# Kernel tuning notes

Measured on AMD Instinct MI355X. Metric: run time of the kernel, lower is better.

Reference implementation:

```python
import jax, jax.numpy as jnp
import numpy as np

L, H = 6, 8          # depth, heads
DM, DH, M = 512, 64, 256  # d_model, d_head, nb random features
EPS = 1e-4


def sinusoidal_pe(n, d, dtype):
    pos = jnp.arange(n, dtype=jnp.float32)[:, None]
    div = jnp.exp(jnp.arange(0, d, 2, dtype=jnp.float32) * (-(np.log(10000.0) / d)))
    pe = jnp.zeros((n, d), jnp.float32)
    pe = pe.at[:, 0::2].set(jnp.sin(pos * div))
    pe = pe.at[:, 1::2].set(jnp.cos(pos * div))
    return pe.astype(dtype)


def layer_norm(x, g, b, eps=1e-5):
    mu = jnp.mean(x, -1, keepdims=True)
    var = jnp.mean(jnp.square(x - mu), -1, keepdims=True)
    return (x - mu) * jax.lax.rsqrt(var + eps) * g + b


def softmax_features(x, proj, is_query):
    # FAVOR+ positive softmax-kernel features. x: [b,h,n,dh], proj: [m,dh]
    dn = DH ** -0.25
    xd = x * dn
    u = jnp.einsum('bhnd,md->bhnm', xd, proj)            # [b,h,n,m]
    diag = 0.5 * jnp.sum(xd * xd, -1, keepdims=True)      # ||x||^2/2 (normalized)
    if is_query:
        stab = jnp.max(u, axis=-1, keepdims=True)
    else:
        stab = jnp.max(u, axis=(-2, -1), keepdims=True)
    return (M ** -0.5) * (jnp.exp(u - diag - stab) + EPS)


def split_heads(t, b, n):
    return t.reshape(b, n, H, DH).transpose(0, 2, 1, 3)   # [b,h,n,dh]


def reference(x, proj, ln1_g, ln1_b, wq, wk, wv, wo, bo, ln2_g, ln2_b, w1, b1, w2, b2):
    b, n, d = x.shape
    x = x + sinusoidal_pe(n, d, x.dtype)[None]
    for i in range(L):
        # --- FAVOR+ linear attention (pre-norm) ---
        h = layer_norm(x, ln1_g[i], ln1_b[i])
        q = split_heads(h @ wq[i], b, n)
        k = split_heads(h @ wk[i], b, n)
        v = split_heads(h @ wv[i], b, n)
        qp = softmax_features(q, proj[i], True)           # [b,h,n,m]
        kp = softmax_features(k, proj[i], False)
        ksum = jnp.sum(kp, axis=2)                         # [b,h,m]
        d_inv = 1.0 / jnp.einsum('bhnm,bhm->bhn', qp, ksum)
        ctx = jnp.einsum('bhnm,bhnd->bhmd', kp, v)         # [b,h,m,dh]
        o = jnp.einsum('bhnm,bhmd->bhnd', qp, ctx) * d_inv[..., None]
        o = o.transpose(0, 2, 1, 3).reshape(b, n, DM)
        x = x + o @ wo[i] + bo[i]
        # --- feed-forward (pre-norm, GELU) ---
        h = layer_norm(x, ln2_g[i], ln2_b[i])
        x = x + jax.nn.gelu(h @ w1[i] + b1[i], approximate=False) @ w2[i] + b2[i]
    return x


def setup_inputs() -> dict:
    key = jax.random.key(0)
    ks = jax.random.split(key, 9)
    s_in = DM ** -0.5
    s_ff = (4 * DM) ** -0.5
    return {
        'x':     jax.random.normal(ks[0], (8, 2048, DM), jnp.float32),
        'proj':  jax.random.normal(ks[1], (L, M, DH), jnp.float32),
        'ln1_g': jnp.ones((L, DM), jnp.float32),
        'ln1_b': jnp.zeros((L, DM), jnp.float32),
        'wq':    jax.random.normal(ks[2], (L, DM, DM), jnp.float32) * s_in,
        'wk':    jax.random.normal(ks[3], (L, DM, DM), jnp.float32) * s_in,
        'wv':    jax.random.normal(ks[4], (L, DM, DM), jnp.float32) * s_in,
        'wo':    jax.random.normal(ks[5], (L, DM, DM), jnp.float32) * s_in,
        'bo':    jnp.zeros((L, DM), jnp.float32),
        'ln2_g': jnp.ones((L, DM), jnp.float32),
        'ln2_b': jnp.zeros((L, DM), jnp.float32),
        'w1':    jax.random.normal(ks[6], (L, DM, 4 * DM), jnp.float32) * s_in,
        'b1':    jnp.zeros((L, 4 * DM), jnp.float32),
        'w2':    jax.random.normal(ks[7], (L, 4 * DM, DM), jnp.float32) * s_ff,
        'b2':    jnp.zeros((L, DM), jnp.float32),
    }
```

## Files before the change

### kernel.cpp

```cpp
#include <hip/hip_runtime.h>
#include <math.h>

#define LNUM 6
#define HNUM 8
#define DMODEL 512
#define DHEAD 64
#define MFEAT 256
#define BATCH 8
#define SEQ 2048
#define TOK (BATCH*SEQ)
#define BHN (BATCH*HNUM)
#define DFF 2048
#define EPSF 1e-4f
#define LN_EPS 1e-5f
#define DNRM 0.35355339059327373f
#define SMF 0.0625f

typedef unsigned short u16;
typedef __attribute__((ext_vector_type(8))) short bf16x8;
typedef __attribute__((ext_vector_type(4))) float f32x4;
#define MFMA16(a,b,c) __builtin_amdgcn_mfma_f32_16x16x32_bf16(a,b,c,0,0,0)

#define GLOAD16(g,l) __builtin_amdgcn_global_load_lds( \
    (const __attribute__((address_space(1))) void*)(g), \
    (__attribute__((address_space(3))) void*)(l), 16, 0, 0)

__device__ __forceinline__ u16 f2bf(float f){
  unsigned int u = __float_as_uint(f);
  u = (u + 0x7fffu + ((u >> 16) & 1u)) >> 16;
  return (u16)u;
}
__device__ __forceinline__ float bf2f(u16 s){
  return __uint_as_float(((unsigned int)s) << 16);
}
__device__ __forceinline__ void atomicMaxF(float* addr, float val){
  if(val >= 0.f) atomicMax((int*)addr, __float_as_int(val));
  else           atomicMin((unsigned int*)addr, __float_as_uint(val));
}
__device__ __forceinline__ float fast_gelu(float z){
  float g2 = z*(1.5957691216f + 0.07135481628f*z*z);
  return z / (1.0f + __expf(-g2));
}

__global__ void k_addpe(const float* __restrict__ x, float* __restrict__ xo){
  int idx = blockIdx.x*256 + threadIdx.x;
  int d = idx & (DMODEL-1);
  int n = (idx >> 9) & (SEQ-1);
  int j = d >> 1;
  float freq = expf((float)(2*j) * (-9.210340371976184f / (float)DMODEL));
  float ang = (float)n * freq;
  float pe = (d & 1) ? cosf(ang) : sinf(ang);
  xo[idx] = x[idx] + pe;
}

__global__ void k_ln(const float* __restrict__ x, const float* __restrict__ g,
                     const float* __restrict__ bv, u16* __restrict__ out){
  __shared__ float sred[8];
  int t = blockIdx.x, tid = threadIdx.x;
  const float2 v = ((const float2*)(x + (size_t)t*DMODEL))[tid];
  float s = v.x + v.y;
  #pragma unroll
  for(int o=32;o;o>>=1) s += __shfl_down(s,o);
  if((tid&63)==0) sred[tid>>6] = s;
  __syncthreads();
  if(tid==0) sred[4] = (sred[0]+sred[1]+sred[2]+sred[3]) * (1.0f/DMODEL);
  __syncthreads();
  float mu = sred[4];
  float dx = v.x - mu, dy = v.y - mu;
  float s2 = dx*dx + dy*dy;
  #pragma unroll
  for(int o=32;o;o>>=1) s2 += __shfl_down(s2,o);
  if((tid&63)==0) sred[tid>>6] = s2;
  __syncthreads();
  if(tid==0) sred[5] = rsqrtf((sred[0]+sred[1]+sred[2]+sred[3])*(1.0f/DMODEL) + LN_EPS);
  __syncthreads();
  float rs = sred[5];
  const float2 gg = ((const float2*)g)[tid];
  const float2 bb = ((const float2*)bv)[tid];
  ushort2 o2; o2.x = f2bf(dx*rs*gg.x + bb.x); o2.y = f2bf(dy*rs*gg.y + bb.y);
  ((ushort2*)(out + (size_t)t*DMODEL))[tid] = o2;
}

__global__ void k_pcvt(const float* __restrict__ p, u16* __restrict__ pb){
  int i = blockIdx.x*256 + threadIdx.x;
  pb[i] = f2bf(p[i]);
}

__global__ void k_wcvt_all(const float* __restrict__ wq, const float* __restrict__ wk,
                           const float* __restrict__ wv, const float* __restrict__ wo,
                           const float* __restrict__ w1, const float* __restrict__ w2,
                           u16* __restrict__ wqT, u16* __restrict__ wkT,
                           u16* __restrict__ wvT, u16* __restrict__ woT,
                           u16* __restrict__ w1T, u16* __restrict__ w2T,
                           float* __restrict__ ksum, float* __restrict__ kmax){
  int bid = blockIdx.x;
  if(bid >= 768){
    int i = (bid-768)*256 + threadIdx.x;
    ksum[i] = 0.f;
    if(i < BHN) kmax[i] = -INFINITY;
    return;
  }
  const float* src; u16* dst; int K, N, bx, by;
  if(bid < 256){
    int which = bid >> 6, sub = bid & 63;
    src = which==0 ? wq : which==1 ? wk : which==2 ? wv : wo;
    dst = which==0 ? wqT : which==1 ? wkT : which==2 ? wvT : woT;
    K = 512; N = 512; bx = sub & 7; by = sub >> 3;
  } else if(bid < 512){
    int sub = bid - 256; src = w1; dst = w1T; K = 512; N = 2048; bx = sub & 31; by = sub >> 5;
  } else {
    int sub = bid - 512; src = w2; dst = w2T; K = 2048; N = 512; bx = sub & 7; by = sub >> 3;
  }
  __shared__ float sm[64][65];
  int kt = by*64, nt = bx*64;
  int t = threadIdx.x, c = t & 63, r4 = t >> 6;
  #pragma unroll
  for(int i=0;i<16;i++){
    int kl = i*4 + r4;
    sm[kl][c] = src[(size_t)(kt+kl)*N + nt + c];
  }
  __syncthreads();
  #pragma unroll
  for(int i=0;i<16;i++){
    int nl = i*4 + r4;
    dst[(size_t)(nt+nl)*K + kt + c] = f2bf(sm[c][nl]);
  }
}

template<int EPI>
__global__ __launch_bounds__(256,4)
void k_mm(const u16* __restrict__ A, const u16* __restrict__ Bt,
          const float* __restrict__ bias, void* __restrict__ Cv,
          int Nc, int K){
  __shared__ u16 As[2][128*32];
  __shared__ u16 Bs[2][128*32];
  int tid = threadIdx.x;
  int w = tid >> 6, lane = tid & 63;
  int wr = w >> 1, wc = w & 1;
  int hi = lane >> 4, li = lane & 15;
  int row0 = blockIdx.y*128, col0 = blockIdx.x*128;
  int lr = lane >> 2;
  int cs = (lane & 3) ^ ((lane >> 3) & 3);
  const u16* gA = A  + (size_t)(row0 + w*16 + lr)*K + cs*8;
  const u16* gB = Bt + (size_t)(col0 + w*16 + lr)*K + cs*8;
  int rb = li*32 + ((hi ^ ((li>>1)&3))<<3);
  f32x4 acc[4][4] = {};

#define STAGE_MM(b,k0) { \
    GLOAD16(gA + (k0),                &As[b][(w*16)*32]);      \
    GLOAD16(gA + (size_t)64*K + (k0), &As[b][(64+w*16)*32]);   \
    GLOAD16(gB + (k0),                &Bs[b][(w*16)*32]);      \
    GLOAD16(gB + (size_t)64*K + (k0), &Bs[b][(64+w*16)*32]); }

  int nk = K >> 5;
  STAGE_MM(0, 0)
  STAGE_MM(1, 32)
  for(int t=0; t<nk; ++t){
    __builtin_amdgcn_sched_barrier(0);
    if(t+1 < nk){ asm volatile("s_waitcnt vmcnt(4)"); }
    else        { asm volatile("s_waitcnt vmcnt(0)"); }
    __builtin_amdgcn_s_barrier();
    __builtin_amdgcn_sched_barrier(0);
    const u16* pa = &As[t&1][0];
    const u16* pb = &Bs[t&1][0];
    bf16x8 bfr[4];
    #pragma unroll
    for(int q=0;q<4;q++) bfr[q] = *(const bf16x8*)&pb[rb + wc*2048 + q*512];
    __builtin_amdgcn_s_setprio(1);
    #pragma unroll
    for(int i2=0;i2<4;i2++){
      bf16x8 a = *(const bf16x8*)&pa[rb + wr*2048 + i2*512];
      #pragma unroll
      for(int j2=0;j2<4;j2++)
        acc[i2][j2] = MFMA16(a, bfr[j2], acc[i2][j2]);
    }
    __builtin_amdgcn_s_setprio(0);
    __builtin_amdgcn_sched_barrier(0);
    __builtin_amdgcn_s_barrier();
    __builtin_amdgcn_sched_barrier(0);
    if(t+2 < nk){ STAGE_MM(t&1, (size_t)(t+2)*32) }
  }
#undef STAGE_MM

  #pragma unroll
  for(int i2=0;i2<4;i2++){
    #pragma unroll
    for(int j2=0;j2<4;j2++){
      int col = col0 + wc*64 + j2*16 + li;
      float bcol = (EPI==2 || EPI==3) ? bias[col] : 0.f;
      if constexpr (EPI==4){
        int nb = row0 + wr*64 + i2*16 + hi*4;
        int b = nb >> 11, n = nb & (SEQ-1);
        int h = col >> 6, dh = col & 63;
        ushort4 pk;
        pk.x = f2bf(acc[i2][j2][0]); pk.y = f2bf(acc[i2][j2][1]);
        pk.z = f2bf(acc[i2][j2][2]); pk.w = f2bf(acc[i2][j2][3]);
        *(ushort4*)((u16*)Cv + (((size_t)(b*HNUM+h)*DHEAD + dh)*SEQ + n)) = pk;
      } else {
        #pragma unroll
        for(int r=0;r<4;r++){
          int row = row0 + wr*64 + i2*16 + hi*4 + r;
          float v = acc[i2][j2][r];
          if constexpr (EPI==1){
            int b = row >> 11, n = row & (SEQ-1);
            int h = col >> 6, dh = col & 63;
            ((u16*)Cv)[((size_t)(b*HNUM+h)*SEQ + n)*DHEAD + dh] = f2bf(v);
          } else if constexpr (EPI==2){
            ((float*)Cv)[(size_t)row*Nc + col] += v + bcol;
          } else {
            ((u16*)Cv)[(size_t)row*Nc + col] = f2bf(fast_gelu(v + bcol));
          }
        }
      }
    }
  }
}

template<int EPI>
__global__ __launch_bounds__(512)
void k_mm8(const u16* __restrict__ A, const u16* __restrict__ Bt,
           const float* __restrict__ bias, void* __restrict__ Cv,
           int Nc, int K){
  __shared__ u16 Ab[3][256*64];
  __shared__ u16 Bb[3][128*64];
  int tid = threadIdx.x;
  int w = tid >> 6, lane = tid & 63;
  int wr = w >> 1, wc = w & 1;
  int hi = lane >> 4, li = lane & 15;
  int row0 = blockIdx.y*256, col0 = blockIdx.x*128;
  int lr = lane >> 3;
  int lc = (lane & 7) ^ lr;
  const u16* gA = A  + (size_t)(row0 + w*8 + lr)*K + lc*8;
  const u16* gB = Bt + (size_t)(col0 + w*8 + lr)*K + lc*8;
  f32x4 acc[4][4] = {};

#define STG8(buf,k0) { \
    GLOAD16(gA + (k0),                  &Ab[buf][w*512]);          \
    GLOAD16(gA + (size_t)64*K  + (k0),  &Ab[buf][4096  + w*512]);  \
    GLOAD16(gA + (size_t)128*K + (k0),  &Ab[buf][8192  + w*512]);  \
    GLOAD16(gA + (size_t)192*K + (k0),  &Ab[buf][12288 + w*512]);  \
    GLOAD16(gB + (k0),                  &Bb[buf][w*512]);          \
    GLOAD16(gB + (size_t)64*K  + (k0),  &Bb[buf][4096  + w*512]); }

  int nk = K >> 6;
  STG8(0, 0)
  STG8(1, 64)
  for(int t=0; t<nk; ++t){
    int buf = t % 3;
    int nbuf = (t+2) % 3;
    size_t nk0 = (size_t)(t+2)*64;
    __builtin_amdgcn_sched_barrier(0);
    if(t+1 < nk){ asm volatile("s_waitcnt vmcnt(6)"); }
    else        { asm volatile("s_waitcnt vmcnt(0)"); }
    __builtin_amdgcn_s_barrier();
    __builtin_amdgcn_sched_barrier(0);
    const u16* pa = &Ab[buf][0];
    const u16* pb = &Bb[buf][0];
    bf16x8 bfr[2][4], af[2][2];
    #pragma unroll
    for(int kk=0;kk<2;kk++){
      int kc = kk*4 + hi;
      #pragma unroll
      for(int j=0;j<4;j++){
        int bc = wc*64 + j*16 + li;
        bfr[kk][j] = *(const bf16x8*)&pb[bc*64 + ((kc ^ (bc&7))<<3)];
      }
      #pragma unroll
      for(int q=0;q<2;q++){
        int ar = wr*64 + q*16 + li;
        af[kk][q] = *(const bf16x8*)&pa[ar*64 + ((kc ^ (ar&7))<<3)];
      }
    }
    if(t+2 < nk){
      GLOAD16(gA + nk0,                  &Ab[nbuf][w*512]);
      GLOAD16(gA + (size_t)64*K  + nk0,  &Ab[nbuf][4096  + w*512]);
      GLOAD16(gA + (size_t)128*K + nk0,  &Ab[nbuf][8192  + w*512]);
    }
    __builtin_amdgcn_s_setprio(1);
    #pragma unroll
    for(int kk=0;kk<2;kk++)
      #pragma unroll
      for(int q=0;q<2;q++)
        #pragma unroll
        for(int j=0;j<4;j++)
          acc[q][j] = MFMA16(af[kk][q], bfr[kk][j], acc[q][j]);
    __builtin_amdgcn_s_setprio(0);
    __builtin_amdgcn_s_barrier();
    bf16x8 af2[2][2];
    #pragma unroll
    for(int kk=0;kk<2;kk++){
      int kc = kk*4 + hi;
      #pragma unroll
      for(int q=0;q<2;q++){
        int ar = wr*64 + (q+2)*16 + li;
        af2[kk][q] = *(const bf16x8*)&pa[ar*64 + ((kc ^ (ar&7))<<3)];
      }
    }
    if(t+2 < nk){
      GLOAD16(gA + (size_t)192*K + nk0,  &Ab[nbuf][12288 + w*512]);
      GLOAD16(gB + nk0,                  &Bb[nbuf][w*512]);
      GLOAD16(gB + (size_t)64*K  + nk0,  &Bb[nbuf][4096  + w*512]);
    }
    __builtin_amdgcn_s_setprio(1);
    #pragma unroll
    for(int kk=0;kk<2;kk++)
      #pragma unroll
      for(int q=0;q<2;q++)
        #pragma unroll
        for(int j=0;j<4;j++)
          acc[q+2][j] = MFMA16(af2[kk][q], bfr[kk][j], acc[q+2][j]);
    __builtin_amdgcn_s_setprio(0);
    __builtin_amdgcn_s_barrier();
  }
#undef STG8

  #pragma unroll
  for(int i2=0;i2<4;i2++){
    #pragma unroll
    for(int j2=0;j2<4;j2++){
      int col = col0 + wc*64 + j2*16 + li;
      float bcol = (EPI==2 || EPI==3) ? bias[col] : 0.f;
      if constexpr (EPI==4){
        int nb = row0 + wr*64 + i2*16 + hi*4;
        int b = nb >> 11, n = nb & (SEQ-1);
        int h = col >> 6, dh = col & 63;
        ushort4 pk;
        pk.x = f2bf(acc[i2][j2][0]); pk.y = f2bf(acc[i2][j2][1]);
        pk.z = f2bf(acc[i2][j2][2]); pk.w = f2bf(acc[i2][j2][3]);
        *(ushort4*)((u16*)Cv + (((size_t)(b*HNUM+h)*DHEAD + dh)*SEQ + n)) = pk;
      } else {
        #pragma unroll
        for(int r=0;r<4;r++){
          int row = row0 + wr*64 + i2*16 + hi*4 + r;
          float v = acc[i2][j2][r];
          if constexpr (EPI==1){
            int b = row >> 11, n = row & (SEQ-1);
            int h = col >> 6, dh = col & 63;
            ((u16*)Cv)[((size_t)(b*HNUM+h)*SEQ + n)*DHEAD + dh] = f2bf(v);
          } else if constexpr (EPI==2){
            ((float*)Cv)[(size_t)row*Nc + col] += v + bcol;
          } else {
            ((u16*)Cv)[(size_t)row*Nc + col] = f2bf(fast_gelu(v + bcol));
          }
        }
      }
    }
  }
}

__global__ __launch_bounds__(256)
void k_kmax(const u16* __restrict__ xg, const u16* __restrict__ pjb,
            float* __restrict__ kmax){
  __shared__ u16 pj[256*64];
  __shared__ u16 xs[128*64];
  __shared__ float wred[4];
  int tid = threadIdx.x, w = tid >> 6, lane = tid & 63;
  int hi = lane >> 4, li = lane & 15;
  int r0 = blockIdx.x * 128;
  int bh = r0 >> 11;
  #pragma unroll
  for(int i=0;i<8;i++){
    int idx = i*256 + tid;
    int m = idx >> 3, c = idx & 7;
    bf16x8 v = *(const bf16x8*)(pjb + m*64 + c*8);
    *(bf16x8*)&pj[m*64 + ((c ^ (m&7))<<3)] = v;
  }
  #pragma unroll
  for(int i=0;i<4;i++){
    int idx = i*256 + tid;
    int m = idx >> 3, c = idx & 7;
    bf16x8 v = *(const bf16x8*)(xg + (size_t)(r0+m)*64 + c*8);
    *(bf16x8*)&xs[m*64 + ((c ^ (m&7))<<3)] = v;
  }
  __syncthreads();
  bf16x8 bfr[2][4];
  #pragma unroll
  for(int ks=0;ks<2;ks++){
    int kc = ks*4 + hi;
    #pragma unroll
    for(int t=0;t<4;t++){
      int bc = w*64 + t*16 + li;
      bfr[ks][t] = *(const bf16x8*)&pj[bc*64 + ((kc ^ (bc&7))<<3)];
    }
  }
  float mx = -1e30f;
  #pragma unroll
  for(int i8=0;i8<8;i8++){
    f32x4 acc[4] = {};
    #pragma unroll
    for(int ks=0;ks<2;ks++){
      int kc = ks*4 + hi;
      int ar = i8*16 + li;
      bf16x8 af = *(const bf16x8*)&xs[ar*64 + ((kc ^ (ar&7))<<3)];
      #pragma unroll
      for(int j2=0;j2<4;j2++)
        acc[j2] = MFMA16(af, bfr[ks][j2], acc[j2]);
    }
    #pragma unroll
    for(int j2=0;j2<4;j2++)
      #pragma unroll
      for(int r=0;r<4;r++) mx = fmaxf(mx, acc[j2][r]);
  }
  #pragma unroll
  for(int o=32;o;o>>=1) mx = fmaxf(mx, __shfl_xor(mx,o));
  if(lane==0) wred[w] = mx;
  __syncthreads();
  if(tid==0){
    float m2 = fmaxf(fmaxf(wred[0],wred[1]), fmaxf(wred[2],wred[3]));
    atomicMaxF(&kmax[bh], m2*DNRM);
  }
}

__global__ __launch_bounds__(256)
void k_kfeat(const u16* __restrict__ xg, const u16* __restrict__ pjb,
             u16* __restrict__ outp, const float* __restrict__ kmax,
             float* __restrict__ ksum){
  __shared__ u16 pj[256*64];
  __shared__ u16 xs[128*64];
  __shared__ float dgs[128];
  int tid = threadIdx.x, w = tid >> 6, lane = tid & 63;
  int hi = lane >> 4, li = lane & 15;
  int r0 = blockIdx.x * 128;
  int bh = r0 >> 11;
  int nbase = r0 & (SEQ-1);
  #pragma unroll
  for(int i=0;i<8;i++){
    int idx = i*256 + tid;
    int m = idx >> 3, c = idx & 7;
    bf16x8 v = *(const bf16x8*)(pjb + m*64 + c*8);
    *(bf16x8*)&pj[m*64 + ((c ^ (m&7))<<3)] = v;
  }
  #pragma unroll
  for(int i=0;i<4;i++){
    int idx = i*256 + tid;
    int m = idx >> 3, c = idx & 7;
    bf16x8 v = *(const bf16x8*)(xg + (size_t)(r0+m)*64 + c*8);
    *(bf16x8*)&xs[m*64 + ((c ^ (m&7))<<3)] = v;
    float s = 0.f;
    #pragma unroll
    for(int j=0;j<8;j++){ float t = bf2f((u16)v[j]); s += t*t; }
    s += __shfl_xor(s,1); s += __shfl_xor(s,2); s += __shfl_xor(s,4);
    if((tid&7)==0) dgs[m] = 0.5f*DNRM*DNRM*s;
  }
  __syncthreads();
  bf16x8 bfr[2][4];
  #pragma unroll
  for(int ks=0;ks<2;ks++){
    int kc = ks*4 + hi;
    #pragma unroll
    for(int t=0;t<4;t++){
      int bc = w*64 + t*16 + li;
      bfr[ks][t] = *(const bf16x8*)&pj[bc*64 + ((kc ^ (bc&7))<<3)];
    }
  }
  float km = kmax[bh];
  float csum[4] = {0.f,0.f,0.f,0.f};
  #pragma unroll
  for(int i8=0;i8<8;i8++){
    f32x4 acc[4] = {};
    #pragma unroll
    for(int ks=0;ks<2;ks++){
      int kc = ks*4 + hi;
      int ar = i8*16 + li;
      bf16x8 af = *(const bf16x8*)&xs[ar*64 + ((kc ^ (ar&7))<<3)];
      #pragma unroll
      for(int j2=0;j2<4;j2++)
        acc[j2] = MFMA16(af, bfr[ks][j2], acc[j2]);
    }
    #pragma unroll
    for(int j2=0;j2<4;j2++){
      int col = w*64 + j2*16 + li;
      ushort4 pk;
      float cpart = 0.f;
      #pragma unroll
      for(int r=0;r<4;r++){
        int rl = i8*16 + hi*4 + r;
        float u = acc[j2][r]*DNRM;
        u16 eb = f2bf(SMF*(__expf(u - dgs[rl] - km) + EPSF));
        ((u16*)&pk)[r] = eb;
        cpart += bf2f(eb);
      }
      *(ushort4*)(outp + ((size_t)(bh*MFEAT + col)*SEQ + nbase + i8*16 + hi*4)) = pk;
      csum[j2] += cpart;
    }
  }
  #pragma unroll
  for(int j2=0;j2<4;j2++){
    float v = csum[j2];
    v += __shfl_xor(v,16); v += __shfl_xor(v,32);
    if(hi==0) atomicAdd(&ksum[bh*MFEAT + w*64 + j2*16 + li], v);
  }
}

__global__ __launch_bounds__(512)
void k_feato(const u16* __restrict__ xg, const u16* __restrict__ pjb,
             const u16* __restrict__ ctxt, const float* __restrict__ ksum,
             u16* __restrict__ o){
  __shared__ u16 smA[16384];
  __shared__ u16 smX[4096];
  __shared__ u16 smQ[64*264];
  __shared__ float dgs[64];
  __shared__ float wred[2][4][32];
  __shared__ float wden[2][4][32];
  __shared__ float ksl[256];
  __shared__ float denl[64];
  int tid = threadIdx.x, w = tid >> 6, lane = tid & 63;
  int hi = lane >> 4, li = lane & 15;
  int g = w >> 2, wq = w & 3;
  int r0 = blockIdx.x * 64;
  int bh = r0 >> 11;
  int b = bh >> 3, h = bh & 7;
  #pragma unroll
  for(int i=0;i<4;i++){
    int idx = i*512 + tid;
    int m = idx >> 3, c = idx & 7;
    bf16x8 v = *(const bf16x8*)(pjb + m*64 + c*8);
    *(bf16x8*)&smA[m*64 + ((c ^ (m&7))<<3)] = v;
  }
  {
    int m = tid >> 3, c = tid & 7;
    bf16x8 v = *(const bf16x8*)(xg + (size_t)(r0+m)*64 + c*8);
    *(bf16x8*)&smX[m*64 + ((c ^ (m&7))<<3)] = v;
    float s = 0.f;
    #pragma unroll
    for(int j=0;j<8;j++){ float t = bf2f((u16)v[j]); s += t*t; }
    s += __shfl_xor(s,1); s += __shfl_xor(s,2); s += __shfl_xor(s,4);
    if((tid&7)==0) dgs[m] = 0.5f*DNRM*DNRM*s;
  }
  if(tid < 256) ksl[tid] = ksum[bh*MFEAT + tid];
  __syncthreads();
  f32x4 acc[2][4] = {};
  #pragma unroll
  for(int ks=0;ks<2;ks++){
    bf16x8 af[2], bfr[4];
    int kc = ks*4 + hi;
    #pragma unroll
    for(int t=0;t<2;t++){
      int ar = g*32 + t*16 + li;
      af[t] = *(const bf16x8*)&smX[ar*64 + ((kc ^ (ar&7))<<3)];
    }
    #pragma unroll
    for(int t=0;t<4;t++){
      int bc = wq*64 + t*16 + li;
      bfr[t] = *(const bf16x8*)&smA[bc*64 + ((kc ^ (bc&7))<<3)];
    }
    #pragma unroll
    for(int i2=0;i2<2;i2++)
      #pragma unroll
      for(int j2=0;j2<4;j2++)
        acc[i2][j2] = MFMA16(af[i2], bfr[j2], acc[i2][j2]);
  }
  __syncthreads();
  {
    int gch = (tid & 31) ^ ((tid >> 5) & 7);
    const u16* gCl = ctxt + (size_t)bh*DHEAD*MFEAT + (size_t)(tid>>5)*MFEAT + gch*8;
    #pragma unroll
    for(int i=0;i<4;i++)
      GLOAD16(gCl + (size_t)i*16*MFEAT, &smA[i*4096 + w*512]);
  }
  #pragma unroll
  for(int i2=0;i2<2;i2++){
    #pragma unroll
    for(int r=0;r<4;r++){
      float v = fmaxf(fmaxf(acc[i2][0][r],acc[i2][1][r]), fmaxf(acc[i2][2][r],acc[i2][3][r]));
      v = fmaxf(v, __shfl_xor(v,1)); v = fmaxf(v, __shfl_xor(v,2));
      v = fmaxf(v, __shfl_xor(v,4)); v = fmaxf(v, __shfl_xor(v,8));
      if(li==0) wred[g][wq][i2*16 + hi*4 + r] = v;
    }
  }
  __builtin_amdgcn_sched_barrier(0);
  asm volatile("s_waitcnt lgkmcnt(0)");
  __builtin_amdgcn_s_barrier();
  __builtin_amdgcn_sched_barrier(0);
  #pragma unroll
  for(int i2=0;i2<2;i2++){
    #pragma unroll
    for(int r=0;r<4;r++){
      int rl = i2*16 + hi*4 + r;
      int row = g*32 + rl;
      float rm = fmaxf(fmaxf(wred[g][0][rl],wred[g][1][rl]),
                       fmaxf(wred[g][2][rl],wred[g][3][rl]));
      float dsum = 0.f;
      #pragma unroll
      for(int j2=0;j2<4;j2++){
        int col = wq*64 + j2*16 + li;
        float u = acc[i2][j2][r]*DNRM;
        u16 eb = f2bf(SMF*(__expf(u - dgs[row] - rm) + EPSF));
        smQ[row*264 + col] = eb;
        dsum += bf2f(eb)*ksl[col];
      }
      dsum += __shfl_xor(dsum,1); dsum += __shfl_xor(dsum,2);
      dsum += __shfl_xor(dsum,4); dsum += __shfl_xor(dsum,8);
      if(li==0) wden[g][wq][rl] = dsum;
    }
  }
  __builtin_amdgcn_sched_barrier(0);
  asm volatile("s_waitcnt vmcnt(0) lgkmcnt(0)");
  __builtin_amdgcn_s_barrier();
  __builtin_amdgcn_sched_barrier(0);
  if(tid < 64){
    int gg = tid >> 5, rr = tid & 31;
    denl[tid] = wden[gg][0][rr]+wden[gg][1][rr]+wden[gg][2][rr]+wden[gg][3][rr];
  }
  int d4 = w >> 1, g2 = w & 1;
  f32x4 acc2[2] = {};
  #pragma unroll
  for(int s=0;s<8;s++){
    int kc = s*4 + hi;
    int bc = d4*16 + li;
    bf16x8 bf = *(const bf16x8*)&smA[bc*256 + ((kc ^ (bc&7))<<3)];
    #pragma unroll
    for(int t=0;t<2;t++){
      int ar = g2*32 + t*16 + li;
      bf16x8 aa = *(const bf16x8*)&smQ[ar*264 + kc*8];
      acc2[t] = MFMA16(aa, bf, acc2[t]);
    }
  }
  __syncthreads();
  int nbase = r0 & (SEQ-1);
  #pragma unroll
  for(int t=0;t<2;t++){
    #pragma unroll
    for(int r=0;r<4;r++){
      int nl = g2*32 + t*16 + hi*4 + r;
      float di = 1.0f/denl[nl];
      o[((size_t)b*SEQ + nbase + nl)*DMODEL + h*DHEAD + d4*16 + li] = f2bf(acc2[t][r]*di);
    }
  }
}

__global__ __launch_bounds__(256)
void k_ctx(const u16* __restrict__ vt, const u16* __restrict__ kpt,
           u16* __restrict__ ctxt){
  __shared__ u16 As[2][64*64];
  __shared__ u16 Bs[2][32*64];
  int tid = threadIdx.x, w = tid >> 6, lane = tid & 63;
  int wr = w >> 1, wc = w & 1;
  int hi = lane >> 4, li = lane & 15;
  int bh = blockIdx.y, mb = blockIdx.x*32;
  int lr = lane >> 3;
  int lc = (lane & 7) ^ lr;
  const u16* gA = vt  + (size_t)bh*DHEAD*SEQ + (size_t)(w*8 + lr)*SEQ + lc*8;
  const u16* gB = kpt + ((size_t)bh*MFEAT + mb + w*8 + lr)*SEQ + lc*8;
  f32x4 acc[2][1] = {};
#define STAGE_CTX(b,k0) { \
    GLOAD16(gA + (k0),                  &As[b][(w*8)*64]);      \
    GLOAD16(gA + (size_t)32*SEQ + (k0), &As[b][(32+w*8)*64]);   \
    GLOAD16(gB + (k0),                  &Bs[b][(w*8)*64]); }
  int nk = SEQ/64;
  STAGE_CTX(0, 0)
  STAGE_CTX(1, 64)
  for(int t=0; t<nk; ++t){
    __builtin_amdgcn_sched_barrier(0);
    if(t+1 < nk){ asm volatile("s_waitcnt vmcnt(3)"); }
    else        { asm volatile("s_waitcnt vmcnt(0)"); }
    __builtin_amdgcn_s_barrier();
    __builtin_amdgcn_sched_barrier(0);
    const u16* pa = &As[t&1][0];
    const u16* pb = &Bs[t&1][0];
    #pragma unroll
    for(int ks=0;ks<2;ks++){
      bf16x8 af[2], bfr;
      int kc = ks*4 + hi;
      #pragma unroll
      for(int q=0;q<2;q++){
        int ar = wr*32 + q*16 + li;
        af[q] = *(const bf16x8*)&pa[ar*64 + ((kc ^ (ar&7))<<3)];
      }
      {
        int bc = wc*16 + li;
        bfr = *(const bf16x8*)&pb[bc*64 + ((kc ^ (bc&7))<<3)];
      }
      __builtin_amdgcn_s_setprio(1);
      #pragma unroll
      for(int i2=0;i2<2;i2++)
        acc[i2][0] = MFMA16(af[i2], bfr, acc[i2][0]);
      __builtin_amdgcn_s_setprio(0);
    }
    __builtin_amdgcn_sched_barrier(0);
    __builtin_amdgcn_s_barrier();
    __builtin_amdgcn_sched_barrier(0);
    if(t+2 < nk){ STAGE_CTX(t&1, (size_t)(t+2)*64) }
  }
#undef STAGE_CTX
  #pragma unroll
  for(int i2=0;i2<2;i2++){
    int m = mb + wc*16 + li;
    #pragma unroll
    for(int r=0;r<4;r++){
      int dh = wr*32 + i2*16 + hi*4 + r;
      ctxt[((size_t)bh*DHEAD + dh)*MFEAT + m] = f2bf(acc[i2][0][r]);
    }
  }
}

extern "C" void kernel_launch(void* const* d_in, const int* in_sizes, int n_in,
                              void* d_out, int out_size, void* d_ws, size_t ws_size,
                              hipStream_t stream){
  (void)in_sizes; (void)n_in; (void)out_size; (void)ws_size;
  const float* x    = (const float*)d_in[0];
  const float* proj = (const float*)d_in[1];
  const float* ln1g = (const float*)d_in[2];
  const float* ln1b = (const float*)d_in[3];
  const float* wq   = (const float*)d_in[4];
  const float* wk   = (const float*)d_in[5];
  const float* wv   = (const float*)d_in[6];
  const float* wo   = (const float*)d_in[7];
  const float* bo   = (const float*)d_in[8];
  const float* ln2g = (const float*)d_in[9];
  const float* ln2b = (const float*)d_in[10];
  const float* w1   = (const float*)d_in[11];
  const float* b1   = (const float*)d_in[12];
  const float* w2   = (const float*)d_in[13];
  const float* b2   = (const float*)d_in[14];
  float* xo = (float*)d_out;

  char* ws = (char*)d_ws;
  u16* bufH  = (u16*)ws;  ws += (size_t)TOK*DMODEL*2;
  u16* bufA  = (u16*)ws;  ws += (size_t)TOK*DMODEL*2;
  u16* featb = (u16*)ws;  ws += (size_t)BHN*SEQ*MFEAT*2;
  u16* ctxt  = (u16*)ws;  ws += (size_t)BHN*DHEAD*MFEAT*2;
  u16* wT    = (u16*)ws;  ws += (size_t)3*1048576*2;
  u16* pjb   = (u16*)ws;  ws += (size_t)LNUM*MFEAT*DHEAD*2;
  float* ksum= (float*)ws; ws += (size_t)BHN*MFEAT*4;
  float* kmax= (float*)ws; ws += 256;

  u16* wqT = wT;
  u16* wkT = wT +  262144;
  u16* wvT = wT +  524288;
  u16* woT = wT +  786432;
  u16* w1T = wT + 1048576;
  u16* w2T = wT + 2097152;

  k_addpe<<<(TOK*DMODEL)/256, 256, 0, stream>>>(x, xo);
  k_pcvt<<<(LNUM*MFEAT*DHEAD)/256, 256, 0, stream>>>(proj, pjb);

  for(int l=0; l<LNUM; l++){
    const u16* pj_l = pjb + (size_t)l*MFEAT*DHEAD;
    k_wcvt_all<<<832, 256, 0, stream>>>(wq + (size_t)l*262144, wk + (size_t)l*262144,
                                        wv + (size_t)l*262144, wo + (size_t)l*262144,
                                        w1 + (size_t)l*1048576, w2 + (size_t)l*1048576,
                                        wqT, wkT, wvT, woT, w1T, w2T, ksum, kmax);
    k_ln<<<TOK, 256, 0, stream>>>(xo, ln1g + l*DMODEL, ln1b + l*DMODEL, bufH);
    k_mm8<1><<<dim3(4,64), 512, 0, stream>>>(bufH, wkT, nullptr, bufA, DMODEL, DMODEL);
    k_kmax<<<(BHN*SEQ)/128, 256, 0, stream>>>(bufA, pj_l, kmax);
    k_kfeat<<<(BHN*SEQ)/128, 256, 0, stream>>>(bufA, pj_l, featb, kmax, ksum);
    k_mm8<4><<<dim3(4,64), 512, 0, stream>>>(bufH, wvT, nullptr, bufA, DMODEL, DMODEL);
    k_ctx<<<dim3(8,BHN), 256, 0, stream>>>(bufA, featb, ctxt);
    k_mm8<1><<<dim3(4,64), 512, 0, stream>>>(bufH, wqT, nullptr, bufA, DMODEL, DMODEL);
    k_feato<<<(BHN*SEQ)/64, 512, 0, stream>>>(bufA, pj_l, ctxt, ksum, bufH);
    k_mm8<2><<<dim3(4,64), 512, 0, stream>>>(bufH, woT, bo + l*DMODEL, xo, DMODEL, DMODEL);
    k_ln<<<TOK, 256, 0, stream>>>(xo, ln2g + l*DMODEL, ln2b + l*DMODEL, bufA);
    k_mm<3><<<dim3(16,128), 256, 0, stream>>>(bufA, w1T, b1 + l*DFF, featb, DFF, DMODEL);
    k_mm<2><<<dim3(4,128), 256, 0, stream>>>(featb, w2T, b2 + l*DMODEL, xo, DMODEL, DFF);
  }
}
```

Baseline: 2.036 ms.

## Fuse key max and projection into one pass, store fp16 logits, exponentiate after

```diff
diff --git a/kernel.cpp b/kernel.cpp
--- a/kernel.cpp
+++ b/kernel.cpp
@@ -33,6 +33,14 @@
 __device__ __forceinline__ float bf2f(u16 s){
   return __uint_as_float(((unsigned int)s) << 16);
 }
+__device__ __forceinline__ u16 f2h(float f){
+  _Float16 h = (_Float16)f;
+  return *(u16*)&h;
+}
+__device__ __forceinline__ float h2f(u16 s){
+  _Float16 h = *(_Float16*)&s;
+  return (float)h;
+}
 __device__ __forceinline__ void atomicMaxF(float* addr, float val){
   if(val >= 0.f) atomicMax((int*)addr, __float_as_int(val));
   else           atomicMin((unsigned int*)addr, __float_as_uint(val));
@@ -92,11 +100,10 @@
                            u16* __restrict__ wqT, u16* __restrict__ wkT,
                            u16* __restrict__ wvT, u16* __restrict__ woT,
                            u16* __restrict__ w1T, u16* __restrict__ w2T,
-                           float* __restrict__ ksum, float* __restrict__ kmax){
+                           float* __restrict__ kmax){
   int bid = blockIdx.x;
   if(bid >= 768){
     int i = (bid-768)*256 + threadIdx.x;
-    ksum[i] = 0.f;
     if(i < BHN) kmax[i] = -INFINITY;
     return;
   }
@@ -349,75 +356,12 @@
 }
 
 __global__ __launch_bounds__(256)
-void k_kmax(const u16* __restrict__ xg, const u16* __restrict__ pjb,
-            float* __restrict__ kmax){
-  __shared__ u16 pj[256*64];
-  __shared__ u16 xs[128*64];
-  __shared__ float wred[4];
-  int tid = threadIdx.x, w = tid >> 6, lane = tid & 63;
-  int hi = lane >> 4, li = lane & 15;
-  int r0 = blockIdx.x * 128;
-  int bh = r0 >> 11;
-  #pragma unroll
-  for(int i=0;i<8;i++){
-    int idx = i*256 + tid;
-    int m = idx >> 3, c = idx & 7;
-    bf16x8 v = *(const bf16x8*)(pjb + m*64 + c*8);
-    *(bf16x8*)&pj[m*64 + ((c ^ (m&7))<<3)] = v;
-  }
-  #pragma unroll
-  for(int i=0;i<4;i++){
-    int idx = i*256 + tid;
-    int m = idx >> 3, c = idx & 7;
-    bf16x8 v = *(const bf16x8*)(xg + (size_t)(r0+m)*64 + c*8);
-    *(bf16x8*)&xs[m*64 + ((c ^ (m&7))<<3)] = v;
-  }
-  __syncthreads();
-  bf16x8 bfr[2][4];
-  #pragma unroll
-  for(int ks=0;ks<2;ks++){
-    int kc = ks*4 + hi;
-    #pragma unroll
-    for(int t=0;t<4;t++){
-      int bc = w*64 + t*16 + li;
-      bfr[ks][t] = *(const bf16x8*)&pj[bc*64 + ((kc ^ (bc&7))<<3)];
-    }
-  }
-  float mx = -1e30f;
-  #pragma unroll
-  for(int i8=0;i8<8;i8++){
-    f32x4 acc[4] = {};
-    #pragma unroll
-    for(int ks=0;ks<2;ks++){
-      int kc = ks*4 + hi;
-      int ar = i8*16 + li;
-      bf16x8 af = *(const bf16x8*)&xs[ar*64 + ((kc ^ (ar&7))<<3)];
-      #pragma unroll
-      for(int j2=0;j2<4;j2++)
-        acc[j2] = MFMA16(af, bfr[ks][j2], acc[j2]);
-    }
-    #pragma unroll
-    for(int j2=0;j2<4;j2++)
-      #pragma unroll
-      for(int r=0;r<4;r++) mx = fmaxf(mx, acc[j2][r]);
-  }
-  #pragma unroll
-  for(int o=32;o;o>>=1) mx = fmaxf(mx, __shfl_xor(mx,o));
-  if(lane==0) wred[w] = mx;
-  __syncthreads();
-  if(tid==0){
-    float m2 = fmaxf(fmaxf(wred[0],wred[1]), fmaxf(wred[2],wred[3]));
-    atomicMaxF(&kmax[bh], m2*DNRM);
-  }
-}
-
-__global__ __launch_bounds__(256)
-void k_kfeat(const u16* __restrict__ xg, const u16* __restrict__ pjb,
-             u16* __restrict__ outp, const float* __restrict__ kmax,
-             float* __restrict__ ksum){
+void k_ku(const u16* __restrict__ xg, const u16* __restrict__ pjb,
+          u16* __restrict__ outp, float* __restrict__ kmax){
   __shared__ u16 pj[256*64];
   __shared__ u16 xs[128*64];
   __shared__ float dgs[128];
+  __shared__ float wred[4];
   int tid = threadIdx.x, w = tid >> 6, lane = tid & 63;
   int hi = lane >> 4, li = lane & 15;
   int r0 = blockIdx.x * 128;
@@ -453,8 +397,7 @@
       bfr[ks][t] = *(const bf16x8*)&pj[bc*64 + ((kc ^ (bc&7))<<3)];
     }
   }
-  float km = kmax[bh];
-  float csum[4] = {0.f,0.f,0.f,0.f};
+  float mx = -1e30f;
   #pragma unroll
   for(int i8=0;i8<8;i8++){
     f32x4 acc[4] = {};
@@ -471,25 +414,49 @@
     for(int j2=0;j2<4;j2++){
       int col = w*64 + j2*16 + li;
       ushort4 pk;
-      float cpart = 0.f;
       #pragma unroll
       for(int r=0;r<4;r++){
         int rl = i8*16 + hi*4 + r;
-        float u = acc[j2][r]*DNRM;
-        u16 eb = f2bf(SMF*(__expf(u - dgs[rl] - km) + EPSF));
-        ((u16*)&pk)[r] = eb;
-        cpart += bf2f(eb);
+        mx = fmaxf(mx, acc[j2][r]);
+        ((u16*)&pk)[r] = f2h(acc[j2][r]*DNRM - dgs[rl]);
       }
       *(ushort4*)(outp + ((size_t)(bh*MFEAT + col)*SEQ + nbase + i8*16 + hi*4)) = pk;
-      csum[j2] += cpart;
-    }
-  }
-  #pragma unroll
-  for(int j2=0;j2<4;j2++){
-    float v = csum[j2];
-    v += __shfl_xor(v,16); v += __shfl_xor(v,32);
-    if(hi==0) atomicAdd(&ksum[bh*MFEAT + w*64 + j2*16 + li], v);
-  }
+    }
+  }
+  #pragma unroll
+  for(int o=32;o;o>>=1) mx = fmaxf(mx, __shfl_xor(mx,o));
+  if(lane==0) wred[w] = mx;
+  __syncthreads();
+  if(tid==0){
+    float m2 = fmaxf(fmaxf(wred[0],wred[1]), fmaxf(wred[2],wred[3]));
+    atomicMaxF(&kmax[bh], m2*DNRM);
+  }
+}
+
+__global__ __launch_bounds__(256)
+void k_kexp(u16* __restrict__ featb, const float* __restrict__ kmax,
+            float* __restrict__ ksum){
+  int row = blockIdx.x*8 + (threadIdx.x >> 5);
+  int l32 = threadIdx.x & 31;
+  float km = kmax[row >> 8];
+  u16* p = featb + (size_t)row*SEQ + l32*64;
+  float s = 0.f;
+  #pragma unroll
+  for(int i=0;i<8;i++){
+    bf16x8 v = *(bf16x8*)(p + i*8);
+    bf16x8 o;
+    #pragma unroll
+    for(int j=0;j<8;j++){
+      float x = h2f((u16)v[j]);
+      u16 eb = f2bf(SMF*(__expf(x - km) + EPSF));
+      o[j] = (short)eb;
+      s += bf2f(eb);
+    }
+    *(bf16x8*)(p + i*8) = o;
+  }
+  s += __shfl_xor(s,1); s += __shfl_xor(s,2); s += __shfl_xor(s,4);
+  s += __shfl_xor(s,8); s += __shfl_xor(s,16);
+  if(l32 == 0) ksum[row] = s;
 }
 
 __global__ __launch_bounds__(512)
@@ -737,14 +704,14 @@
 
   for(int l=0; l<LNUM; l++){
     const u16* pj_l = pjb + (size_t)l*MFEAT*DHEAD;
-    k_wcvt_all<<<832, 256, 0, stream>>>(wq + (size_t)l*262144, wk + (size_t)l*262144,
+    k_wcvt_all<<<769, 256, 0, stream>>>(wq + (size_t)l*262144, wk + (size_t)l*262144,
                                         wv + (size_t)l*262144, wo + (size_t)l*262144,
                                         w1 + (size_t)l*1048576, w2 + (size_t)l*1048576,
-                                        wqT, wkT, wvT, woT, w1T, w2T, ksum, kmax);
+                                        wqT, wkT, wvT, woT, w1T, w2T, kmax);
     k_ln<<<TOK, 256, 0, stream>>>(xo, ln1g + l*DMODEL, ln1b + l*DMODEL, bufH);
     k_mm8<1><<<dim3(4,64), 512, 0, stream>>>(bufH, wkT, nullptr, bufA, DMODEL, DMODEL);
-    k_kmax<<<(BHN*SEQ)/128, 256, 0, stream>>>(bufA, pj_l, kmax);
-    k_kfeat<<<(BHN*SEQ)/128, 256, 0, stream>>>(bufA, pj_l, featb, kmax, ksum);
+    k_ku<<<(BHN*SEQ)/128, 256, 0, stream>>>(bufA, pj_l, featb, kmax);
+    k_kexp<<<(BHN*MFEAT)/8, 256, 0, stream>>>(featb, kmax, ksum);
     k_mm8<4><<<dim3(4,64), 512, 0, stream>>>(bufH, wvT, nullptr, bufA, DMODEL, DMODEL);
     k_ctx<<<dim3(8,BHN), 256, 0, stream>>>(bufA, featb, ctxt);
     k_mm8<1><<<dim3(4,64), 512, 0, stream>>>(bufH, wqT, nullptr, bufA, DMODEL, DMODEL);
```

New measurement: 2.201 ms. 1.08x slower.
